# Kernel tuning notes

Hardware: AMD Instinct MI355X
Metric: run time of the kernel (lower is better)

Reference implementation:

```python
import jax, jax.numpy as jnp
import numpy as np

LATENT = 2048
PROJ = 128
N = 4096
TEMP = 0.5
BN_EPS = 1e-5
COS_EPS = 1e-8


def _batchnorm(x, gamma=None, beta=None):
    # training-mode BatchNorm1d: biased batch stats
    mean = jnp.mean(x, axis=0)
    var = jnp.mean((x - mean) ** 2, axis=0)
    xn = (x - mean) * jax.lax.rsqrt(var + BN_EPS)
    if gamma is not None:
        xn = xn * gamma + beta
    return xn


def _project(h, W1, gamma1, beta1, W2):
    x = h @ W1.T                      # [N, latent]
    x = jax.nn.relu(_batchnorm(x, gamma1, beta1))
    x = x @ W2.T                      # [N, proj]
    return _batchnorm(x)              # bn2 affine=False


def _normalize(z):
    n = jnp.linalg.norm(z, axis=-1, keepdims=True)
    return z / jnp.maximum(n, COS_EPS)


def setup_inputs() -> dict:
    key = jax.random.key(0)
    ks = jax.random.split(key, 4)
    scale_w1 = 1.0 / np.sqrt(LATENT)
    return {
        "h1": jax.random.normal(ks[0], (N, LATENT), jnp.float32),
        "h2": jax.random.normal(ks[1], (N, LATENT), jnp.float32),
        "W1": jax.random.normal(ks[2], (LATENT, LATENT), jnp.float32) * scale_w1,
        "gamma1": jnp.ones((LATENT,), jnp.float32),
        "beta1": jnp.zeros((LATENT,), jnp.float32),
        "W2": jax.random.normal(ks[3], (PROJ, LATENT), jnp.float32) * scale_w1,
    }


def reference(h1, h2, W1, gamma1, beta1, W2):
    z1 = _project(h1, W1, gamma1, beta1, W2)
    z2 = _project(h2, W1, gamma1, beta1, W2)
    zn1 = _normalize(z1)
    zn2 = _normalize(z2)
    inv_t = 1.0 / TEMP
    # cosine similarity as normalized GEMMs (same math as broadcast cossim)
    sim11 = (zn1 @ zn1.T) * inv_t      # [N, N]
    sim22 = (zn2 @ zn2.T) * inv_t
    sim12 = (zn1 @ zn2.T) * inv_t
    d = sim12.shape[-1]
    eye = jnp.eye(d, dtype=bool)
    neg_inf = jnp.float32(-jnp.inf)
    sim11 = jnp.where(eye, neg_inf, sim11)
    sim22 = jnp.where(eye, neg_inf, sim22)
    raw_scores1 = jnp.concatenate([sim12, sim11], axis=-1)       # [N, 2N]
    raw_scores2 = jnp.concatenate([sim22, sim12.T], axis=-1)     # [N, 2N]
    raw_scores = jnp.concatenate([raw_scores1, raw_scores2], axis=-2)  # [2N, 2N]
    targets = jnp.arange(2 * d, dtype=jnp.int64 if jax.config.jax_enable_x64 else jnp.int32)
    return raw_scores, targets
```

## Files before the change

kernel.cpp:

```cpp
#include <hip/hip_runtime.h>
#include <hip/hip_bf16.h>
#include <math.h>

#define NROWS 4096
#define MTOT  8192
#define LATENT 2048
#define PROJ 128
#define OUTN 8192
#define SPLITK 4
#define CH1 128
#define CH2 64

using bf16 = __hip_bfloat16;
using bf16x8 = __attribute__((ext_vector_type(8))) short;
using bf16x4 = __attribute__((ext_vector_type(4))) short;
using f32x4  = __attribute__((ext_vector_type(4))) float;

#define LDS_AS(p) ((__attribute__((address_space(3))) void*)(p))
#define GLB_AS(p) ((const __attribute__((address_space(1))) void*)(p))

__device__ __forceinline__ float bf2f(short s) {
    return __uint_as_float(((unsigned)(unsigned short)s) << 16);
}
__device__ __forceinline__ short f2bf(float f) {
    bf16 h = __float2bfloat16(f);
    return __builtin_bit_cast(short, h);
}

__global__ void conv_h_kern(const float* __restrict__ h1, const float* __restrict__ h2,
                            bf16* __restrict__ out)
{
    const size_t e = ((size_t)blockIdx.x * 256 + threadIdx.x) * 8;
    const size_t HALF = (size_t)NROWS * LATENT;
    const float* src = (e < HALF) ? (h1 + e) : (h2 + (e - HALF));
    const float4 v0 = *reinterpret_cast<const float4*>(src);
    const float4 v1 = *reinterpret_cast<const float4*>(src + 4);
    bf16x8 o;
    o[0] = f2bf(v0.x); o[1] = f2bf(v0.y); o[2] = f2bf(v0.z); o[3] = f2bf(v0.w);
    o[4] = f2bf(v1.x); o[5] = f2bf(v1.y); o[6] = f2bf(v1.z); o[7] = f2bf(v1.w);
    *reinterpret_cast<bf16x8*>(out + e) = o;
}

__global__ void conv_w_kern(const float* __restrict__ W1, const float* __restrict__ W2,
                            bf16* __restrict__ W1b, bf16* __restrict__ W2b)
{
    const size_t e = ((size_t)blockIdx.x * 256 + threadIdx.x) * 8;
    const size_t W1N = (size_t)LATENT * LATENT;
    const float* src; bf16* dst; size_t off;
    if (e < W1N) { src = W1; dst = W1b; off = e; }
    else         { src = W2; dst = W2b; off = e - W1N; }
    const float4 v0 = *reinterpret_cast<const float4*>(src + off);
    const float4 v1 = *reinterpret_cast<const float4*>(src + off + 4);
    bf16x8 o;
    o[0] = f2bf(v0.x); o[1] = f2bf(v0.y); o[2] = f2bf(v0.z); o[3] = f2bf(v0.w);
    o[4] = f2bf(v1.x); o[5] = f2bf(v1.y); o[6] = f2bf(v1.z); o[7] = f2bf(v1.w);
    *reinterpret_cast<bf16x8*>(dst + off) = o;
}

#define AREG(buf,kh) (sm + ((buf)*2 + (kh)) * 16384)
#define BREG(buf,kh) (sm + 65536 + ((buf)*2 + (kh)) * 16384)

#define LDA_(buf,kh,m) (*reinterpret_cast<const bf16x8*>(AREG(buf,kh) + (wr*128 + (m)*16 + fr)*64 + rslot))
#define LDB_(buf,kh,n) (*reinterpret_cast<const bf16x8*>(BREG(buf,kh) + (wc*64  + (n)*16 + fr)*64 + rslot))

#define STAGE_A(buf,kh,kt) do { \
    const bf16* g_ = Ag + (size_t)(bm + w*16 + srow) * 2048 + (kt)*64 + (kh)*32 + selem; \
    __builtin_amdgcn_global_load_lds(GLB_AS(g_),                  LDS_AS(AREG(buf,kh) + w*1024),        16, 0, 0); \
    __builtin_amdgcn_global_load_lds(GLB_AS(g_ + (size_t)128*2048), LDS_AS(AREG(buf,kh) + 8192 + w*1024), 16, 0, 0); \
} while(0)

#define STAGE_B(buf,kh,kt) do { \
    const bf16* g_ = Bg + (size_t)(bn + w*16 + srow) * 2048 + (kt)*64 + (kh)*32 + selem; \
    __builtin_amdgcn_global_load_lds(GLB_AS(g_),                  LDS_AS(BREG(buf,kh) + w*1024),        16, 0, 0); \
    __builtin_amdgcn_global_load_lds(GLB_AS(g_ + (size_t)128*2048), LDS_AS(BREG(buf,kh) + 8192 + w*1024), 16, 0, 0); \
} while(0)

#define PH(bufi, khi, mb, READB, STAGE_STMT, DO_VMCNT) do { \
    if (READB) { b0 = LDB_(bufi,khi,0); b1 = LDB_(bufi,khi,1); b2 = LDB_(bufi,khi,2); b3 = LDB_(bufi,khi,3); } \
    bf16x8 a0 = LDA_(bufi,khi,(mb)+0), a1 = LDA_(bufi,khi,(mb)+1), a2 = LDA_(bufi,khi,(mb)+2), a3 = LDA_(bufi,khi,(mb)+3); \
    STAGE_STMT; \
    __builtin_amdgcn_s_barrier(); \
    asm volatile("s_waitcnt lgkmcnt(0)" ::: "memory"); \
    __builtin_amdgcn_sched_barrier(0); \
    __builtin_amdgcn_s_setprio(1); \
    acc[(mb)+0][0] = __builtin_amdgcn_mfma_f32_16x16x32_bf16(b0, a0, acc[(mb)+0][0], 0,0,0); \
    acc[(mb)+0][1] = __builtin_amdgcn_mfma_f32_16x16x32_bf16(b1, a0, acc[(mb)+0][1], 0,0,0); \
    acc[(mb)+0][2] = __builtin_amdgcn_mfma_f32_16x16x32_bf16(b2, a0, acc[(mb)+0][2], 0,0,0); \
    acc[(mb)+0][3] = __builtin_amdgcn_mfma_f32_16x16x32_bf16(b3, a0, acc[(mb)+0][3], 0,0,0); \
    acc[(mb)+1][0] = __builtin_amdgcn_mfma_f32_16x16x32_bf16(b0, a1, acc[(mb)+1][0], 0,0,0); \
    acc[(mb)+1][1] = __builtin_amdgcn_mfma_f32_16x16x32_bf16(b1, a1, acc[(mb)+1][1], 0,0,0); \
    acc[(mb)+1][2] = __builtin_amdgcn_mfma_f32_16x16x32_bf16(b2, a1, acc[(mb)+1][2], 0,0,0); \
    acc[(mb)+1][3] = __builtin_amdgcn_mfma_f32_16x16x32_bf16(b3, a1, acc[(mb)+1][3], 0,0,0); \
    acc[(mb)+2][0] = __builtin_amdgcn_mfma_f32_16x16x32_bf16(b0, a2, acc[(mb)+2][0], 0,0,0); \
    acc[(mb)+2][1] = __builtin_amdgcn_mfma_f32_16x16x32_bf16(b1, a2, acc[(mb)+2][1], 0,0,0); \
    acc[(mb)+2][2] = __builtin_amdgcn_mfma_f32_16x16x32_bf16(b2, a2, acc[(mb)+2][2], 0,0,0); \
    acc[(mb)+2][3] = __builtin_amdgcn_mfma_f32_16x16x32_bf16(b3, a2, acc[(mb)+2][3], 0,0,0); \
    acc[(mb)+3][0] = __builtin_amdgcn_mfma_f32_16x16x32_bf16(b0, a3, acc[(mb)+3][0], 0,0,0); \
    acc[(mb)+3][1] = __builtin_amdgcn_mfma_f32_16x16x32_bf16(b1, a3, acc[(mb)+3][1], 0,0,0); \
    acc[(mb)+3][2] = __builtin_amdgcn_mfma_f32_16x16x32_bf16(b2, a3, acc[(mb)+3][2], 0,0,0); \
    acc[(mb)+3][3] = __builtin_amdgcn_mfma_f32_16x16x32_bf16(b3, a3, acc[(mb)+3][3], 0,0,0); \
    __builtin_amdgcn_s_setprio(0); \
    if (DO_VMCNT) { asm volatile("s_waitcnt vmcnt(6)" ::: "memory"); } \
    __builtin_amdgcn_s_barrier(); \
    __builtin_amdgcn_sched_barrier(0); \
} while (0)

__global__ __launch_bounds__(512, 2)
void gemm1_256(const bf16* __restrict__ Ag, const bf16* __restrict__ Bg,
               bf16* __restrict__ C)
{
    extern __shared__ __align__(16) char sm[];

    const int t    = threadIdx.x;
    const int lane = t & 63;
    const int w    = t >> 6;
    const int wr   = w >> 2;
    const int wc   = w & 3;

    const int bid = blockIdx.x;
    const int lin = (bid & 7) * 32 + (bid >> 3);
    const int bm  = (lin >> 3) * 256;
    const int bn  = (lin & 7) * 256;

    const int srow  = lane >> 2;
    const int selem = 8 * ((lane & 3) ^ ((lane >> 2) & 3));
    const int fr    = lane & 15;
    const int rslot = 16 * ((lane >> 4) ^ (lane & 3));

    f32x4 acc[8][4];
#pragma unroll
    for (int m = 0; m < 8; ++m)
#pragma unroll
        for (int n = 0; n < 4; ++n)
#pragma unroll
            for (int r = 0; r < 4; ++r) acc[m][n][r] = 0.f;

    bf16x8 b0, b1, b2, b3;

    STAGE_B(0,0,0); STAGE_A(0,0,0); STAGE_B(0,1,0); STAGE_A(0,1,0);
    STAGE_B(1,0,1); STAGE_A(1,0,1); STAGE_B(1,1,1);
    asm volatile("s_waitcnt vmcnt(6)" ::: "memory");
    __builtin_amdgcn_s_barrier();
    __builtin_amdgcn_sched_barrier(0);

    for (int i = 0; i < 15; ++i) {
        const int kt1 = 2*i + 1, kt2 = 2*i + 2, kt3 = 2*i + 3;
        PH(0,0, 0, true,  STAGE_A(1,1,kt1), false);
        PH(0,0, 4, false, STAGE_B(0,0,kt2), false);
        PH(0,1, 0, true,  STAGE_A(0,0,kt2), false);
        PH(0,1, 4, false, STAGE_B(0,1,kt2), true);
        PH(1,0, 0, true,  STAGE_A(0,1,kt2), false);
        PH(1,0, 4, false, STAGE_B(1,0,kt3), false);
        PH(1,1, 0, true,  STAGE_A(1,0,kt3), false);
        PH(1,1, 4, false, STAGE_B(1,1,kt3), true);
    }

    STAGE_A(1,1,31);
    asm volatile("s_waitcnt vmcnt(0)" ::: "memory");
    __builtin_amdgcn_s_barrier();
    __builtin_amdgcn_sched_barrier(0);
    PH(0,0, 0, true,  ((void)0), false);
    PH(0,0, 4, false, ((void)0), false);
    PH(0,1, 0, true,  ((void)0), false);
    PH(0,1, 4, false, ((void)0), false);
    PH(1,0, 0, true,  ((void)0), false);
    PH(1,0, 4, false, ((void)0), false);
    PH(1,1, 0, true,  ((void)0), false);
    PH(1,1, 4, false, ((void)0), false);

    const int j_l = (lane >> 4) * 4;
#pragma unroll
    for (int m = 0; m < 8; ++m)
#pragma unroll
        for (int n = 0; n < 4; ++n) {
            const int crow = bm + wr * 128 + m * 16 + fr;
            const int ccol = bn + wc * 64 + n * 16 + j_l;
            bf16x4 o;
#pragma unroll
            for (int r = 0; r < 4; ++r) o[r] = f2bf(acc[m][n][r]);
            *reinterpret_cast<bf16x4*>(&C[(size_t)crow * LATENT + ccol]) = o;
        }
}

__global__ __launch_bounds__(256)
void gemm2_splitk(const bf16* __restrict__ A, const bf16* __restrict__ B,
                  float* __restrict__ Part)
{
    __shared__ __align__(16) bf16 As[128 * 32];
    __shared__ __align__(16) bf16 Bs[128 * 32];

    const int kc = blockIdx.x;
    const int bm = blockIdx.y * 128;

    const int t    = threadIdx.x;
    const int lane = t & 63;
    const int w    = t >> 6;
    const int wr   = w >> 1;
    const int wc   = w & 1;
    const int lrow = lane >> 2;
    const int lcol = (lane & 3) * 8;

    f32x4 acc[4][4];
#pragma unroll
    for (int m = 0; m < 4; ++m)
#pragma unroll
        for (int n = 0; n < 4; ++n)
#pragma unroll
            for (int r = 0; r < 4; ++r) acc[m][n][r] = 0.f;

    const int fr = lane & 15;
    const int fk = (lane >> 4) * 8;
    const int kbeg = kc * (LATENT / SPLITK);
    const int kend = kbeg + (LATENT / SPLITK);

    for (int k0 = kbeg; k0 < kend; k0 += 32) {
#pragma unroll
        for (int q = 0; q < 2; ++q) {
            const int chunk = w * 2 + q;
            const int row = chunk * 16 + lrow;
            __builtin_amdgcn_global_load_lds(
                GLB_AS(&A[(size_t)(bm + row) * LATENT + k0 + lcol]),
                LDS_AS(&As[chunk * 512]), 16, 0, 0);
            __builtin_amdgcn_global_load_lds(
                GLB_AS(&B[(size_t)row * LATENT + k0 + lcol]),
                LDS_AS(&Bs[chunk * 512]), 16, 0, 0);
        }
        __syncthreads();

        bf16x8 a[4], b[4];
#pragma unroll
        for (int m = 0; m < 4; ++m)
            a[m] = *reinterpret_cast<const bf16x8*>(&As[(wr * 64 + m * 16 + fr) * 32 + fk]);
#pragma unroll
        for (int n = 0; n < 4; ++n)
            b[n] = *reinterpret_cast<const bf16x8*>(&Bs[(wc * 64 + n * 16 + fr) * 32 + fk]);

#pragma unroll
        for (int m = 0; m < 4; ++m)
#pragma unroll
            for (int n = 0; n < 4; ++n)
                acc[m][n] = __builtin_amdgcn_mfma_f32_16x16x32_bf16(b[n], a[m], acc[m][n], 0, 0, 0);
        __syncthreads();
    }

    const int i_l = lane & 15;
    const int j_l = (lane >> 4) * 4;
#pragma unroll
    for (int m = 0; m < 4; ++m)
#pragma unroll
        for (int n = 0; n < 4; ++n) {
            const int crow = bm + wr * 64 + m * 16 + i_l;
            const int ccol = wc * 64 + n * 16 + j_l;
            *reinterpret_cast<float4*>(&Part[((size_t)kc * MTOT + crow) * PROJ + ccol]) =
                make_float4(acc[m][n][0], acc[m][n][1], acc[m][n][2], acc[m][n][3]);
        }
}

__global__ void splitk_reduce(const float* __restrict__ Part, float* __restrict__ Z)
{
    const size_t i = ((size_t)blockIdx.x * 256 + threadIdx.x) * 4;
    float4 s = *reinterpret_cast<const float4*>(Part + i);
#pragma unroll
    for (int kc = 1; kc < SPLITK; ++kc) {
        const float4 v = *reinterpret_cast<const float4*>(Part + (size_t)kc * MTOT * PROJ + i);
        s.x += v.x; s.y += v.y; s.z += v.z; s.w += v.w;
    }
    *reinterpret_cast<float4*>(Z + i) = s;
}

__global__ __launch_bounds__(256)
void stats1_partial(const bf16* __restrict__ X, float* __restrict__ pS, float* __restrict__ pSS)
{
    const int c0    = threadIdx.x * 8;
    const int chunk = blockIdx.x;
    const int half  = blockIdx.y;
    const int r0    = half * NROWS + chunk * (NROWS / CH1);
    float s[8], ss[8];
#pragma unroll
    for (int j = 0; j < 8; ++j) { s[j] = 0.f; ss[j] = 0.f; }
    for (int r = r0; r < r0 + NROWS / CH1; ++r) {
        const bf16x8 v = *reinterpret_cast<const bf16x8*>(&X[(size_t)r * LATENT + c0]);
#pragma unroll
        for (int j = 0; j < 8; ++j) {
            const float f = bf2f(v[j]);
            s[j] += f;
            ss[j] = fmaf(f, f, ss[j]);
        }
    }
    const size_t o = ((size_t)(half * CH1 + chunk)) * LATENT + c0;
#pragma unroll
    for (int j = 0; j < 8; ++j) { pS[o + j] = s[j]; pSS[o + j] = ss[j]; }
}

__global__ void stats1_final(const float* __restrict__ pS, const float* __restrict__ pSS,
                             float* __restrict__ mean, float* __restrict__ rstd)
{
    const int c    = blockIdx.x * 256 + threadIdx.x;
    const int half = blockIdx.y;
    float s = 0.f, ss = 0.f;
    for (int i = 0; i < CH1; ++i) {
        s  += pS [((size_t)(half * CH1 + i)) * LATENT + c];
        ss += pSS[((size_t)(half * CH1 + i)) * LATENT + c];
    }
    const float m   = s / NROWS;
    const float var = ss / NROWS - m * m;
    mean[half * LATENT + c] = m;
    rstd[half * LATENT + c] = 1.0f / sqrtf(var + 1e-5f);
}

__global__ void bn1_apply_relu_bf16(bf16* __restrict__ X,
                                    const float* __restrict__ mean, const float* __restrict__ rstd,
                                    const float* __restrict__ gamma, const float* __restrict__ beta)
{
    const size_t idx = (size_t)blockIdx.x * 256 + threadIdx.x;
    const size_t e   = idx * 8;
    const int c      = (int)(e & (LATENT - 1));
    const int half   = (int)(e >> 23);
    const int sc     = half * LATENT + c;
    const bf16x8 v = *reinterpret_cast<const bf16x8*>(X + e);
    const float4 m0 = *reinterpret_cast<const float4*>(mean + sc);
    const float4 m1 = *reinterpret_cast<const float4*>(mean + sc + 4);
    const float4 r0 = *reinterpret_cast<const float4*>(rstd + sc);
    const float4 r1 = *reinterpret_cast<const float4*>(rstd + sc + 4);
    const float4 g0 = *reinterpret_cast<const float4*>(gamma + c);
    const float4 g1 = *reinterpret_cast<const float4*>(gamma + c + 4);
    const float4 b0 = *reinterpret_cast<const float4*>(beta + c);
    const float4 b1 = *reinterpret_cast<const float4*>(beta + c + 4);
    const float mm[8] = {m0.x, m0.y, m0.z, m0.w, m1.x, m1.y, m1.z, m1.w};
    const float rr[8] = {r0.x, r0.y, r0.z, r0.w, r1.x, r1.y, r1.z, r1.w};
    const float gg[8] = {g0.x, g0.y, g0.z, g0.w, g1.x, g1.y, g1.z, g1.w};
    const float bb[8] = {b0.x, b0.y, b0.z, b0.w, b1.x, b1.y, b1.z, b1.w};
    bf16x8 o;
#pragma unroll
    for (int j = 0; j < 8; ++j) {
        const float f = fmaxf(fmaf((bf2f(v[j]) - mm[j]) * rr[j], gg[j], bb[j]), 0.f);
        o[j] = f2bf(f);
    }
    *reinterpret_cast<bf16x8*>(X + e) = o;
}

__global__ __launch_bounds__(128)
void stats2_partial(const float* __restrict__ Z, float* __restrict__ pS, float* __restrict__ pSS)
{
    const int c     = threadIdx.x;
    const int chunk = blockIdx.x;
    const int half  = blockIdx.y;
    const int r0    = half * NROWS + chunk * (NROWS / CH2);
    float s = 0.f, ss = 0.f;
    for (int r = r0; r < r0 + NROWS / CH2; ++r) {
        const float v = Z[(size_t)r * PROJ + c];
        s += v;
        ss = fmaf(v, v, ss);
    }
    pS [(size_t)(half * CH2 + chunk) * PROJ + c] = s;
    pSS[(size_t)(half * CH2 + chunk) * PROJ + c] = ss;
}

__global__ __launch_bounds__(128)
void stats2_final(const float* __restrict__ pS, const float* __restrict__ pSS,
                  float* __restrict__ mean, float* __restrict__ rstd)
{
    const int c    = threadIdx.x;
    const int half = blockIdx.x;
    float s = 0.f, ss = 0.f;
    for (int i = 0; i < CH2; ++i) {
        s  += pS [(size_t)(half * CH2 + i) * PROJ + c];
        ss += pSS[(size_t)(half * CH2 + i) * PROJ + c];
    }
    const float m   = s / NROWS;
    const float var = ss / NROWS - m * m;
    mean[half * PROJ + c] = m;
    rstd[half * PROJ + c] = 1.0f / sqrtf(var + 1e-5f);
}

__global__ __launch_bounds__(64)
void bn2_normalize_bf16(const float* __restrict__ Z,
                        const float* __restrict__ mean, const float* __restrict__ rstd,
                        bf16* __restrict__ Zn, int* __restrict__ tgt)
{
    const int row  = blockIdx.x;
    const int half = row >> 12;
    const int lane = threadIdx.x;
    const float* zr = Z + (size_t)row * PROJ;
    const float v0 = (zr[lane]      - mean[half * PROJ + lane])      * rstd[half * PROJ + lane];
    const float v1 = (zr[lane + 64] - mean[half * PROJ + lane + 64]) * rstd[half * PROJ + lane + 64];
    float ss = v0 * v0 + v1 * v1;
#pragma unroll
    for (int o = 32; o > 0; o >>= 1) ss += __shfl_xor(ss, o);
    const float inv = 1.0f / fmaxf(sqrtf(ss), 1e-8f);
    bf16* orow = Zn + (size_t)row * PROJ;
    orow[lane]      = __float2bfloat16(v0 * inv);
    orow[lane + 64] = __float2bfloat16(v1 * inv);
    if (lane == 0) tgt[row] = row;
}

__global__ __launch_bounds__(256)
void sim_bf16(const bf16* __restrict__ zn, float* __restrict__ out)
{
    __shared__ __align__(16) bf16 As[4 * 128 * 32];
    __shared__ __align__(16) bf16 Bs[4 * 128 * 32];

    const int t    = threadIdx.x;
    const int lane = t & 63;
    const int w    = t >> 6;
    const int wr   = w >> 1;
    const int wc   = w & 1;
    const int bi   = blockIdx.y * 128;
    const int bj   = blockIdx.x * 128;

    const bf16* Ub = zn + (size_t)bi * PROJ;
    const bf16* Vb = zn + (size_t)(bj ^ 4096) * PROJ;

    const int srow = t >> 2;
    const int ske  = (t & 3) * 8;

#pragma unroll
    for (int q = 0; q < 4; ++q)
#pragma unroll
        for (int h = 0; h < 2; ++h) {
            const int row = h * 64 + srow;
            const int ke  = q * 32 + ske;
            __builtin_amdgcn_global_load_lds(
                GLB_AS(&Ub[(size_t)row * PROJ + ke]),
                LDS_AS(&As[q * 4096 + h * 2048 + srow * 32 + ske]), 16, 0, 0);
            __builtin_amdgcn_global_load_lds(
                GLB_AS(&Vb[(size_t)row * PROJ + ke]),
                LDS_AS(&Bs[q * 4096 + h * 2048 + srow * 32 + ske]), 16, 0, 0);
        }
    __syncthreads();

    f32x4 acc[4][4];
#pragma unroll
    for (int m = 0; m < 4; ++m)
#pragma unroll
        for (int n = 0; n < 4; ++n)
#pragma unroll
            for (int r = 0; r < 4; ++r) acc[m][n][r] = 0.f;

    const int fr = lane & 15;
    const int fk = (lane >> 4) * 8;

#pragma unroll
    for (int q = 0; q < 4; ++q) {
        bf16x8 a[4], b[4];
#pragma unroll
        for (int m = 0; m < 4; ++m)
            a[m] = *reinterpret_cast<const bf16x8*>(&As[q * 4096 + (wr * 64 + m * 16 + fr) * 32 + fk]);
#pragma unroll
        for (int n = 0; n < 4; ++n)
            b[n] = *reinterpret_cast<const bf16x8*>(&Bs[q * 4096 + (wc * 64 + n * 16 + fr) * 32 + fk]);
#pragma unroll
        for (int m = 0; m < 4; ++m)
#pragma unroll
            for (int n = 0; n < 4; ++n)
                acc[m][n] = __builtin_amdgcn_mfma_f32_16x16x32_bf16(b[n], a[m], acc[m][n], 0, 0, 0);
    }

    const int i_l = lane & 15;
    const int j_l = (lane >> 4) * 4;
#pragma unroll
    for (int m = 0; m < 4; ++m)
#pragma unroll
        for (int n = 0; n < 4; ++n) {
            const int gi  = bi + wr * 64 + m * 16 + i_l;
            const int gj0 = bj + wc * 64 + n * 16 + j_l;
            float v[4];
#pragma unroll
            for (int r = 0; r < 4; ++r) v[r] = acc[m][n][r] * 2.0f;
            const int mj = (gi ^ 4096) - gj0;
            if (mj >= 0 && mj < 4) v[mj] = -1.0e30f;
            *reinterpret_cast<float4*>(&out[(size_t)gi * OUTN + gj0]) =
                make_float4(v[0], v[1], v[2], v[3]);
        }
}

extern "C" void kernel_launch(void* const* d_in, const int* in_sizes, int n_in,
                              void* d_out, int out_size, void* d_ws, size_t ws_size,
                              hipStream_t stream)
{
    const float* h1 = (const float*)d_in[0];
    const float* h2 = (const float*)d_in[1];
    const float* W1 = (const float*)d_in[2];
    const float* g1 = (const float*)d_in[3];
    const float* b1 = (const float*)d_in[4];
    const float* W2 = (const float*)d_in[5];
    float* out = (float*)d_out;

    char* p = (char*)d_ws;
    auto carve = [&](size_t bytes) { char* r = p; p += (bytes + 255) & ~(size_t)255; return r; };
    bf16*  W1b   = (bf16*) carve((size_t)LATENT * LATENT * 2);
    bf16*  W2b   = (bf16*) carve((size_t)PROJ * LATENT * 2);
    bf16*  hb    = (bf16*) carve((size_t)MTOT * LATENT * 2);
    bf16*  X     = (bf16*) carve((size_t)MTOT * LATENT * 2);
    float* Part  = (float*)carve((size_t)SPLITK * MTOT * PROJ * 4);
    float* Z     = (float*)carve((size_t)MTOT * PROJ * 4);
    bf16*  znb   = (bf16*) carve((size_t)MTOT * PROJ * 2);
    float* pS    = (float*)carve((size_t)2 * CH1 * LATENT * 4);
    float* pSS   = (float*)carve((size_t)2 * CH1 * LATENT * 4);
    float* mean1 = (float*)carve(2 * LATENT * 4);
    float* rstd1 = (float*)carve(2 * LATENT * 4);
    float* mean2 = (float*)carve(2 * PROJ * 4);
    float* rstd2 = (float*)carve(2 * PROJ * 4);

    conv_w_kern<<<dim3((LATENT * LATENT + PROJ * LATENT) / 2048), 256, 0, stream>>>(W1, W2, W1b, W2b);
    conv_h_kern<<<dim3(MTOT * LATENT / 2048), 256, 0, stream>>>(h1, h2, hb);

    gemm1_256<<<dim3(256), 512, 131072, stream>>>(hb, W1b, X);

    stats1_partial<<<dim3(CH1, 2), 256, 0, stream>>>(X, pS, pSS);
    stats1_final<<<dim3(LATENT / 256, 2), 256, 0, stream>>>(pS, pSS, mean1, rstd1);
    bn1_apply_relu_bf16<<<dim3(MTOT * LATENT / 2048), 256, 0, stream>>>(X, mean1, rstd1, g1, b1);

    gemm2_splitk<<<dim3(SPLITK, MTOT / 128), 256, 0, stream>>>(X, W2b, Part);
    splitk_reduce<<<dim3(MTOT * PROJ / 1024), 256, 0, stream>>>(Part, Z);

    stats2_partial<<<dim3(CH2, 2), 128, 0, stream>>>(Z, pS, pSS);
    stats2_final<<<dim3(2), 128, 0, stream>>>(pS, pSS, mean2, rstd2);
    int* tgt = (int*)(out + (size_t)OUTN * OUTN);
    bn2_normalize_bf16<<<dim3(MTOT), 64, 0, stream>>>(Z, mean2, rstd2, znb, tgt);

    sim_bf16<<<dim3(OUTN / 128, OUTN / 128), 256, 0, stream>>>(znb, out);
}
```

Baseline: 248.3 us.

## Fuse BN1 stats into GEMM1 epilogue, merge conversions and split-K reduce with BN2 stats

The four fp32-to-bf16 conversions now run in one launch, and the GEMM1 epilogue computes per-column sums and sums of squares from its fp32 accumulators. That removes the separate stats1 pass that re-read the whole activation matrix. Split-K for GEMM2 goes from 4 to 8, and the split-K reduction is fused with the BN2 statistics. The bn2 normalise kernel packs 4 rows per block, and the similarity output uses non-temporal stores. The fused statistics are taken from fp32 accumulators rather than bf16-rounded values, so numerics shift slightly. The larger split-K also increases the partial-sum traffic.

```diff
diff --git a/kernel.cpp b/kernel.cpp
--- a/kernel.cpp
+++ b/kernel.cpp
@@ -7,9 +7,8 @@
 #define LATENT 2048
 #define PROJ 128
 #define OUTN 8192
-#define SPLITK 4
-#define CH1 128
-#define CH2 64
+#define SPLITK 8
+#define CH2 128
 
 using bf16 = __hip_bfloat16;
 using bf16x8 = __attribute__((ext_vector_type(8))) short;
@@ -27,28 +26,20 @@
     return __builtin_bit_cast(short, h);
 }
 
-__global__ void conv_h_kern(const float* __restrict__ h1, const float* __restrict__ h2,
-                            bf16* __restrict__ out)
-{
-    const size_t e = ((size_t)blockIdx.x * 256 + threadIdx.x) * 8;
-    const size_t HALF = (size_t)NROWS * LATENT;
-    const float* src = (e < HALF) ? (h1 + e) : (h2 + (e - HALF));
-    const float4 v0 = *reinterpret_cast<const float4*>(src);
-    const float4 v1 = *reinterpret_cast<const float4*>(src + 4);
-    bf16x8 o;
-    o[0] = f2bf(v0.x); o[1] = f2bf(v0.y); o[2] = f2bf(v0.z); o[3] = f2bf(v0.w);
-    o[4] = f2bf(v1.x); o[5] = f2bf(v1.y); o[6] = f2bf(v1.z); o[7] = f2bf(v1.w);
-    *reinterpret_cast<bf16x8*>(out + e) = o;
-}
-
-__global__ void conv_w_kern(const float* __restrict__ W1, const float* __restrict__ W2,
-                            bf16* __restrict__ W1b, bf16* __restrict__ W2b)
-{
-    const size_t e = ((size_t)blockIdx.x * 256 + threadIdx.x) * 8;
-    const size_t W1N = (size_t)LATENT * LATENT;
+__global__ void conv_all(const float* __restrict__ W1, const float* __restrict__ W2,
+                         const float* __restrict__ h1, const float* __restrict__ h2,
+                         bf16* __restrict__ W1b, bf16* __restrict__ W2b,
+                         bf16* __restrict__ hb)
+{
+    const size_t g = ((size_t)blockIdx.x * 256 + threadIdx.x) * 8;
+    const size_t N_W1 = (size_t)LATENT * LATENT;
+    const size_t N_W2 = (size_t)PROJ * LATENT;
+    const size_t N_H  = (size_t)NROWS * LATENT;
     const float* src; bf16* dst; size_t off;
-    if (e < W1N) { src = W1; dst = W1b; off = e; }
-    else         { src = W2; dst = W2b; off = e - W1N; }
+    if (g < N_W1)                  { src = W1; dst = W1b;       off = g; }
+    else if (g < N_W1 + N_W2)      { src = W2; dst = W2b;       off = g - N_W1; }
+    else if (g < N_W1 + N_W2 + N_H){ src = h1; dst = hb;        off = g - N_W1 - N_W2; }
+    else                           { src = h2; dst = hb + N_H;  off = g - N_W1 - N_W2 - N_H; }
     const float4 v0 = *reinterpret_cast<const float4*>(src + off);
     const float4 v1 = *reinterpret_cast<const float4*>(src + off + 4);
     bf16x8 o;
@@ -107,7 +98,7 @@
 
 __global__ __launch_bounds__(512, 2)
 void gemm1_256(const bf16* __restrict__ Ag, const bf16* __restrict__ Bg,
-               bf16* __restrict__ C)
+               bf16* __restrict__ C, float* __restrict__ pS1, float* __restrict__ pSS1)
 {
     extern __shared__ __align__(16) char sm[];
 
@@ -180,116 +171,30 @@
             for (int r = 0; r < 4; ++r) o[r] = f2bf(acc[m][n][r]);
             *reinterpret_cast<bf16x4*>(&C[(size_t)crow * LATENT + ccol]) = o;
         }
-}
-
-__global__ __launch_bounds__(256)
-void gemm2_splitk(const bf16* __restrict__ A, const bf16* __restrict__ B,
-                  float* __restrict__ Part)
-{
-    __shared__ __align__(16) bf16 As[128 * 32];
-    __shared__ __align__(16) bf16 Bs[128 * 32];
-
-    const int kc = blockIdx.x;
-    const int bm = blockIdx.y * 128;
-
-    const int t    = threadIdx.x;
-    const int lane = t & 63;
-    const int w    = t >> 6;
-    const int wr   = w >> 1;
-    const int wc   = w & 1;
-    const int lrow = lane >> 2;
-    const int lcol = (lane & 3) * 8;
-
-    f32x4 acc[4][4];
-#pragma unroll
-    for (int m = 0; m < 4; ++m)
-#pragma unroll
-        for (int n = 0; n < 4; ++n)
-#pragma unroll
-            for (int r = 0; r < 4; ++r) acc[m][n][r] = 0.f;
-
-    const int fr = lane & 15;
-    const int fk = (lane >> 4) * 8;
-    const int kbeg = kc * (LATENT / SPLITK);
-    const int kend = kbeg + (LATENT / SPLITK);
-
-    for (int k0 = kbeg; k0 < kend; k0 += 32) {
-#pragma unroll
-        for (int q = 0; q < 2; ++q) {
-            const int chunk = w * 2 + q;
-            const int row = chunk * 16 + lrow;
-            __builtin_amdgcn_global_load_lds(
-                GLB_AS(&A[(size_t)(bm + row) * LATENT + k0 + lcol]),
-                LDS_AS(&As[chunk * 512]), 16, 0, 0);
-            __builtin_amdgcn_global_load_lds(
-                GLB_AS(&B[(size_t)row * LATENT + k0 + lcol]),
-                LDS_AS(&Bs[chunk * 512]), 16, 0, 0);
+
+#pragma unroll
+    for (int n = 0; n < 4; ++n)
+#pragma unroll
+        for (int r = 0; r < 4; ++r) {
+            float sv = 0.f, qv = 0.f;
+#pragma unroll
+            for (int m = 0; m < 8; ++m) {
+                const float v = acc[m][n][r];
+                sv += v;
+                qv = fmaf(v, v, qv);
+            }
+#pragma unroll
+            for (int o = 1; o < 16; o <<= 1) {
+                sv += __shfl_xor(sv, o);
+                qv += __shfl_xor(qv, o);
+            }
+            if (fr == 0) {
+                const int slot = ((bm >> 8) << 1) + wr;
+                const int col  = bn + wc * 64 + n * 16 + j_l + r;
+                pS1 [(size_t)slot * LATENT + col] = sv;
+                pSS1[(size_t)slot * LATENT + col] = qv;
+            }
         }
-        __syncthreads();
-
-        bf16x8 a[4], b[4];
-#pragma unroll
-        for (int m = 0; m < 4; ++m)
-            a[m] = *reinterpret_cast<const bf16x8*>(&As[(wr * 64 + m * 16 + fr) * 32 + fk]);
-#pragma unroll
-        for (int n = 0; n < 4; ++n)
-            b[n] = *reinterpret_cast<const bf16x8*>(&Bs[(wc * 64 + n * 16 + fr) * 32 + fk]);
-
-#pragma unroll
-        for (int m = 0; m < 4; ++m)
-#pragma unroll
-            for (int n = 0; n < 4; ++n)
-                acc[m][n] = __builtin_amdgcn_mfma_f32_16x16x32_bf16(b[n], a[m], acc[m][n], 0, 0, 0);
-        __syncthreads();
-    }
-
-    const int i_l = lane & 15;
-    const int j_l = (lane >> 4) * 4;
-#pragma unroll
-    for (int m = 0; m < 4; ++m)
-#pragma unroll
-        for (int n = 0; n < 4; ++n) {
-            const int crow = bm + wr * 64 + m * 16 + i_l;
-            const int ccol = wc * 64 + n * 16 + j_l;
-            *reinterpret_cast<float4*>(&Part[((size_t)kc * MTOT + crow) * PROJ + ccol]) =
-                make_float4(acc[m][n][0], acc[m][n][1], acc[m][n][2], acc[m][n][3]);
-        }
-}
-
-__global__ void splitk_reduce(const float* __restrict__ Part, float* __restrict__ Z)
-{
-    const size_t i = ((size_t)blockIdx.x * 256 + threadIdx.x) * 4;
-    float4 s = *reinterpret_cast<const float4*>(Part + i);
-#pragma unroll
-    for (int kc = 1; kc < SPLITK; ++kc) {
-        const float4 v = *reinterpret_cast<const float4*>(Part + (size_t)kc * MTOT * PROJ + i);
-        s.x += v.x; s.y += v.y; s.z += v.z; s.w += v.w;
-    }
-    *reinterpret_cast<float4*>(Z + i) = s;
-}
-
-__global__ __launch_bounds__(256)
-void stats1_partial(const bf16* __restrict__ X, float* __restrict__ pS, float* __restrict__ pSS)
-{
-    const int c0    = threadIdx.x * 8;
-    const int chunk = blockIdx.x;
-    const int half  = blockIdx.y;
-    const int r0    = half * NROWS + chunk * (NROWS / CH1);
-    float s[8], ss[8];
-#pragma unroll
-    for (int j = 0; j < 8; ++j) { s[j] = 0.f; ss[j] = 0.f; }
-    for (int r = r0; r < r0 + NROWS / CH1; ++r) {
-        const bf16x8 v = *reinterpret_cast<const bf16x8*>(&X[(size_t)r * LATENT + c0]);
-#pragma unroll
-        for (int j = 0; j < 8; ++j) {
-            const float f = bf2f(v[j]);
-            s[j] += f;
-            ss[j] = fmaf(f, f, ss[j]);
-        }
-    }
-    const size_t o = ((size_t)(half * CH1 + chunk)) * LATENT + c0;
-#pragma unroll
-    for (int j = 0; j < 8; ++j) { pS[o + j] = s[j]; pSS[o + j] = ss[j]; }
 }
 
 __global__ void stats1_final(const float* __restrict__ pS, const float* __restrict__ pSS,
@@ -298,9 +203,9 @@
     const int c    = blockIdx.x * 256 + threadIdx.x;
     const int half = blockIdx.y;
     float s = 0.f, ss = 0.f;
-    for (int i = 0; i < CH1; ++i) {
-        s  += pS [((size_t)(half * CH1 + i)) * LATENT + c];
-        ss += pSS[((size_t)(half * CH1 + i)) * LATENT + c];
+    for (int i = 0; i < 32; ++i) {
+        s  += pS [((size_t)(half * 32 + i)) * LATENT + c];
+        ss += pSS[((size_t)(half * 32 + i)) * LATENT + c];
     }
     const float m   = s / NROWS;
     const float var = ss / NROWS - m * m;
@@ -339,21 +244,99 @@
     *reinterpret_cast<bf16x8*>(X + e) = o;
 }
 
+__global__ __launch_bounds__(256)
+void gemm2_splitk(const bf16* __restrict__ A, const bf16* __restrict__ B,
+                  float* __restrict__ Part)
+{
+    __shared__ __align__(16) bf16 As[128 * 32];
+    __shared__ __align__(16) bf16 Bs[128 * 32];
+
+    const int kc = blockIdx.x;
+    const int bm = blockIdx.y * 128;
+
+    const int t    = threadIdx.x;
+    const int lane = t & 63;
+    const int w    = t >> 6;
+    const int wr   = w >> 1;
+    const int wc   = w & 1;
+    const int lrow = lane >> 2;
+    const int lcol = (lane & 3) * 8;
+
+    f32x4 acc[4][4];
+#pragma unroll
+    for (int m = 0; m < 4; ++m)
+#pragma unroll
+        for (int n = 0; n < 4; ++n)
+#pragma unroll
+            for (int r = 0; r < 4; ++r) acc[m][n][r] = 0.f;
+
+    const int fr = lane & 15;
+    const int fk = (lane >> 4) * 8;
+    const int kbeg = kc * (LATENT / SPLITK);
+    const int kend = kbeg + (LATENT / SPLITK);
+
+    for (int k0 = kbeg; k0 < kend; k0 += 32) {
+#pragma unroll
+        for (int q = 0; q < 2; ++q) {
+            const int chunk = w * 2 + q;
+            const int row = chunk * 16 + lrow;
+            __builtin_amdgcn_global_load_lds(
+                GLB_AS(&A[(size_t)(bm + row) * LATENT + k0 + lcol]),
+                LDS_AS(&As[chunk * 512]), 16, 0, 0);
+            __builtin_amdgcn_global_load_lds(
+                GLB_AS(&B[(size_t)row * LATENT + k0 + lcol]),
+                LDS_AS(&Bs[chunk * 512]), 16, 0, 0);
+        }
+        __syncthreads();
+
+        bf16x8 a[4], b[4];
+#pragma unroll
+        for (int m = 0; m < 4; ++m)
+            a[m] = *reinterpret_cast<const bf16x8*>(&As[(wr * 64 + m * 16 + fr) * 32 + fk]);
+#pragma unroll
+        for (int n = 0; n < 4; ++n)
+            b[n] = *reinterpret_cast<const bf16x8*>(&Bs[(wc * 64 + n * 16 + fr) * 32 + fk]);
+
+#pragma unroll
+        for (int m = 0; m < 4; ++m)
+#pragma unroll
+            for (int n = 0; n < 4; ++n)
+                acc[m][n] = __builtin_amdgcn_mfma_f32_16x16x32_bf16(b[n], a[m], acc[m][n], 0, 0, 0);
+        __syncthreads();
+    }
+
+    const int i_l = lane & 15;
+    const int j_l = (lane >> 4) * 4;
+#pragma unroll
+    for (int m = 0; m < 4; ++m)
+#pragma unroll
+        for (int n = 0; n < 4; ++n) {
+            const int crow = bm + wr * 64 + m * 16 + i_l;
+            const int ccol = wc * 64 + n * 16 + j_l;
+            *reinterpret_cast<float4*>(&Part[((size_t)kc * MTOT + crow) * PROJ + ccol]) =
+                make_float4(acc[m][n][0], acc[m][n][1], acc[m][n][2], acc[m][n][3]);
+        }
+}
+
 __global__ __launch_bounds__(128)
-void stats2_partial(const float* __restrict__ Z, float* __restrict__ pS, float* __restrict__ pSS)
+void reduce2_kern(const float* __restrict__ Part, float* __restrict__ Z,
+                  float* __restrict__ pS2, float* __restrict__ pSS2)
 {
     const int c     = threadIdx.x;
     const int chunk = blockIdx.x;
-    const int half  = blockIdx.y;
-    const int r0    = half * NROWS + chunk * (NROWS / CH2);
+    const int r0    = chunk * (MTOT / CH2);
     float s = 0.f, ss = 0.f;
-    for (int r = r0; r < r0 + NROWS / CH2; ++r) {
-        const float v = Z[(size_t)r * PROJ + c];
-        s += v;
-        ss = fmaf(v, v, ss);
-    }
-    pS [(size_t)(half * CH2 + chunk) * PROJ + c] = s;
-    pSS[(size_t)(half * CH2 + chunk) * PROJ + c] = ss;
+    for (int r = r0; r < r0 + MTOT / CH2; ++r) {
+        float z = 0.f;
+#pragma unroll
+        for (int kc = 0; kc < SPLITK; ++kc)
+            z += Part[((size_t)kc * MTOT + r) * PROJ + c];
+        Z[(size_t)r * PROJ + c] = z;
+        s += z;
+        ss = fmaf(z, z, ss);
+    }
+    pS2 [(size_t)chunk * PROJ + c] = s;
+    pSS2[(size_t)chunk * PROJ + c] = ss;
 }
 
 __global__ __launch_bounds__(128)
@@ -363,9 +346,9 @@
     const int c    = threadIdx.x;
     const int half = blockIdx.x;
     float s = 0.f, ss = 0.f;
-    for (int i = 0; i < CH2; ++i) {
-        s  += pS [(size_t)(half * CH2 + i) * PROJ + c];
-        ss += pSS[(size_t)(half * CH2 + i) * PROJ + c];
+    for (int i = 0; i < CH2 / 2; ++i) {
+        s  += pS [(size_t)(half * (CH2 / 2) + i) * PROJ + c];
+        ss += pSS[(size_t)(half * (CH2 / 2) + i) * PROJ + c];
     }
     const float m   = s / NROWS;
     const float var = ss / NROWS - m * m;
@@ -373,14 +356,14 @@
     rstd[half * PROJ + c] = 1.0f / sqrtf(var + 1e-5f);
 }
 
-__global__ __launch_bounds__(64)
+__global__ __launch_bounds__(256)
 void bn2_normalize_bf16(const float* __restrict__ Z,
                         const float* __restrict__ mean, const float* __restrict__ rstd,
                         bf16* __restrict__ Zn, int* __restrict__ tgt)
 {
-    const int row  = blockIdx.x;
+    const int row  = blockIdx.x * 4 + (threadIdx.x >> 6);
     const int half = row >> 12;
-    const int lane = threadIdx.x;
+    const int lane = threadIdx.x & 63;
     const float* zr = Z + (size_t)row * PROJ;
     const float v0 = (zr[lane]      - mean[half * PROJ + lane])      * rstd[half * PROJ + lane];
     const float v1 = (zr[lane + 64] - mean[half * PROJ + lane + 64]) * rstd[half * PROJ + lane + 64];
@@ -464,13 +447,13 @@
         for (int n = 0; n < 4; ++n) {
             const int gi  = bi + wr * 64 + m * 16 + i_l;
             const int gj0 = bj + wc * 64 + n * 16 + j_l;
-            float v[4];
+            f32x4 v;
 #pragma unroll
             for (int r = 0; r < 4; ++r) v[r] = acc[m][n][r] * 2.0f;
             const int mj = (gi ^ 4096) - gj0;
             if (mj >= 0 && mj < 4) v[mj] = -1.0e30f;
-            *reinterpret_cast<float4*>(&out[(size_t)gi * OUTN + gj0]) =
-                make_float4(v[0], v[1], v[2], v[3]);
+            __builtin_nontemporal_store(
+                v, reinterpret_cast<f32x4*>(&out[(size_t)gi * OUTN + gj0]));
         }
 }
 
@@ -495,29 +478,29 @@
     float* Part  = (float*)carve((size_t)SPLITK * MTOT * PROJ * 4);
     float* Z     = (float*)carve((size_t)MTOT * PROJ * 4);
     bf16*  znb   = (bf16*) carve((size_t)MTOT * PROJ * 2);
-    float* pS    = (float*)carve((size_t)2 * CH1 * LATENT * 4);
-    float* pSS   = (float*)carve((size_t)2 * CH1 * LATENT * 4);
+    float* pS1   = (float*)carve((size_t)64 * LATENT * 4);
+    float* pSS1  = (float*)carve((size_t)64 * LATENT * 4);
+    float* pS2   = (float*)carve((size_t)CH2 * PROJ * 4);
+    float* pSS2  = (float*)carve((size_t)CH2 * PROJ * 4);
     float* mean1 = (float*)carve(2 * LATENT * 4);
     float* rstd1 = (float*)carve(2 * LATENT * 4);
     float* mean2 = (float*)carve(2 * PROJ * 4);
     float* rstd2 = (float*)carve(2 * PROJ * 4);
 
-    conv_w_kern<<<dim3((LATENT * LATENT + PROJ * LATENT) / 2048), 256, 0, stream>>>(W1, W2, W1b, W2b);
-    conv_h_kern<<<dim3(MTOT * LATENT / 2048), 256, 0, stream>>>(h1, h2, hb);
-
-    gemm1_256<<<dim3(256), 512, 131072, stream>>>(hb, W1b, X);
-
-    stats1_partial<<<dim3(CH1, 2), 256, 0, stream>>>(X, pS, pSS);
-    stats1_final<<<dim3(LATENT / 256, 2), 256, 0, stream>>>(pS, pSS, mean1, rstd1);
+    const int conv_groups = (LATENT * LATENT + PROJ * LATENT + 2 * NROWS * LATENT) / 8;
+    conv_all<<<dim3(conv_groups / 256), 256, 0, stream>>>(W1, W2, h1, h2, W1b, W2b, hb);
+
+    gemm1_256<<<dim3(256), 512, 131072, stream>>>(hb, W1b, X, pS1, pSS1);
+
+    stats1_final<<<dim3(LATENT / 256, 2), 256, 0, stream>>>(pS1, pSS1, mean1, rstd1);
     bn1_apply_relu_bf16<<<dim3(MTOT * LATENT / 2048), 256, 0, stream>>>(X, mean1, rstd1, g1, b1);
 
     gemm2_splitk<<<dim3(SPLITK, MTOT / 128), 256, 0, stream>>>(X, W2b, Part);
-    splitk_reduce<<<dim3(MTOT * PROJ / 1024), 256, 0, stream>>>(Part, Z);
-
-    stats2_partial<<<dim3(CH2, 2), 128, 0, stream>>>(Z, pS, pSS);
-    stats2_final<<<dim3(2), 128, 0, stream>>>(pS, pSS, mean2, rstd2);
+    reduce2_kern<<<dim3(CH2), 128, 0, stream>>>(Part, Z, pS2, pSS2);
+    stats2_final<<<dim3(2), 128, 0, stream>>>(pS2, pSS2, mean2, rstd2);
+
     int* tgt = (int*)(out + (size_t)OUTN * OUTN);
-    bn2_normalize_bf16<<<dim3(MTOT), 64, 0, stream>>>(Z, mean2, rstd2, znb, tgt);
+    bn2_normalize_bf16<<<dim3(MTOT / 4), 256, 0, stream>>>(Z, mean2, rstd2, znb, tgt);
 
     sim_bf16<<<dim3(OUTN / 128, OUTN / 128), 256, 0, stream>>>(znb, out);
 }
```

Measured after the change: 231.8 us. -6.7%, faster.
